# Optimization experiments

Measured on AMD Instinct MI355X. Metric: run time of the kernel, lower is better.

## Reference

```python
import jax, jax.numpy as jnp
import numpy as np

PAD_IDX, EOS_IDX, SOS_IDX = 0, 1, 2
NEG = -10000.0


def setup_inputs() -> dict:
    key = jax.random.key(0)
    k1, k2, k3 = jax.random.split(key, 3)
    B, T, K = 64, 2048, 256
    y = jax.random.normal(k1, (B, T, K), dtype=jnp.float32)
    # transition matrix initialized as in crf.__init__
    trans = jax.random.normal(k2, (K, K), dtype=jnp.float32)
    trans = trans.at[SOS_IDX, :].set(NEG)
    trans = trans.at[:, EOS_IDX].set(NEG)
    trans = trans.at[:, PAD_IDX].set(NEG)
    trans = trans.at[PAD_IDX, :].set(NEG)
    trans = trans.at[PAD_IDX, EOS_IDX].set(0.0)
    trans = trans.at[PAD_IDX, PAD_IDX].set(0.0)
    # variable-length float mask (1.0 for valid steps), as the module expects
    lengths = jax.random.randint(k3, (B,), T // 2, T + 1)
    mask = (jnp.arange(T)[None, :] < lengths[:, None]).astype(jnp.float32)
    return {"y": y, "mask": mask, "trans": trans}


def reference(y, mask, trans):
    # Linear-chain CRF partition function (forward algorithm in log space).
    # new_score[b,i] = y[b,t,i] + logsumexp_j(score[b,j] + trans[i,j])
    B, T, K = y.shape
    score0 = jnp.full((B, K), NEG, dtype=y.dtype).at[:, SOS_IDX].set(0.0)

    def step(score, xs):
        emit_t, mask_t = xs  # [B,K], [B]
        # score[b,None,j] + trans[None,i,j] -> lse over j
        new = emit_t + jax.scipy.special.logsumexp(
            score[:, None, :] + trans[None, :, :], axis=-1)
        m = mask_t[:, None]
        score = new * m + score * (1.0 - m)
        return score, None

    score, _ = jax.lax.scan(step, score0,
                            (jnp.swapaxes(y, 0, 1), mask.T))  # scan over T
    return jax.scipy.special.logsumexp(score, axis=-1)  # [B]
```

## Files before the change

kernel.cpp:

```cpp
#include <hip/hip_runtime.h>


typedef _Float16 f16x8 __attribute__((ext_vector_type(8)));
typedef _Float16 f16x4 __attribute__((ext_vector_type(4)));
typedef float    f32x4 __attribute__((ext_vector_type(4)));

#define TT 2048
#define KK 256
#define NB 16
#define NTH 512
#define SOS_IDX 2

#define MFMA(A, B, C) __builtin_amdgcn_mfma_f32_16x16x32_f16((A), (B), (C), 0, 0, 0)

__global__ __launch_bounds__(NTH, 2)
void crf_fwd_kernel(const float* __restrict__ y, const float* __restrict__ mask,
                    const float* __restrict__ trans, float* __restrict__ out)
{
    const int tid = threadIdx.x;
    const int w = tid >> 6, l = tid & 63;
    const int c = l & 15;
    const int s = l >> 4;
    const int sw = (c & 7) << 4;
    const int bb = blockIdx.x * NB;

    __shared__ __align__(16) char  Vlds[2][NB * 512];
    __shared__ __align__(16) float sred[2][NB][12];
    __shared__ float Lcs[NB];

    f16x8 af0[8], af1[8];
    {
        const float* t0 = trans + (size_t)(32 * w + c) * KK + 8 * s;
        const float* t1 = t0 + 16 * KK;
        #pragma unroll
        for (int kt = 0; kt < 8; ++kt) {
            float4 a0 = *(const float4*)(t0 + 32 * kt);
            float4 a1 = *(const float4*)(t0 + 32 * kt + 4);
            float4 b0 = *(const float4*)(t1 + 32 * kt);
            float4 b1 = *(const float4*)(t1 + 32 * kt + 4);
            f16x8 A, Bv;
            A[0] = (_Float16)__expf(a0.x); A[1] = (_Float16)__expf(a0.y);
            A[2] = (_Float16)__expf(a0.z); A[3] = (_Float16)__expf(a0.w);
            A[4] = (_Float16)__expf(a1.x); A[5] = (_Float16)__expf(a1.y);
            A[6] = (_Float16)__expf(a1.z); A[7] = (_Float16)__expf(a1.w);
            Bv[0] = (_Float16)__expf(b0.x); Bv[1] = (_Float16)__expf(b0.y);
            Bv[2] = (_Float16)__expf(b0.z); Bv[3] = (_Float16)__expf(b0.w);
            Bv[4] = (_Float16)__expf(b1.x); Bv[5] = (_Float16)__expf(b1.y);
            Bv[6] = (_Float16)__expf(b1.z); Bv[7] = (_Float16)__expf(b1.w);
            af0[kt] = A; af1[kt] = Bv;
        }
    }

    {
        const int cq = tid >> 5, q = tid & 31;
        const float* mrow = mask + (size_t)(bb + cq) * TT;
        float ls = 0.f;
        #pragma unroll
        for (int i = 0; i < TT / 32; ++i) ls += mrow[q + 32 * i];
        #pragma unroll
        for (int off = 16; off >= 1; off >>= 1) ls += __shfl_xor(ls, off, 64);
        if (q == 0) Lcs[cq] = ls;
    }

    const int r0 = 32 * w + 4 * s;
    float W0 = (r0 + 0 == SOS_IDX) ? 1.f : 0.f;
    float W1 = (r0 + 1 == SOS_IDX) ? 1.f : 0.f;
    float W2 = (r0 + 2 == SOS_IDX) ? 1.f : 0.f;
    float W3 = (r0 + 3 == SOS_IDX) ? 1.f : 0.f;
    float W4 = (r0 + 16 == SOS_IDX) ? 1.f : 0.f;
    float W5 = (r0 + 17 == SOS_IDX) ? 1.f : 0.f;
    float W6 = (r0 + 18 == SOS_IDX) ? 1.f : 0.f;
    float W7 = (r0 + 19 == SOS_IDX) ? 1.f : 0.f;
    {
        char* wb = Vlds[0] + (c << 9);
        f16x4 h0 = {(_Float16)W0, (_Float16)W1, (_Float16)W2, (_Float16)W3};
        f16x4 h1 = {(_Float16)W4, (_Float16)W5, (_Float16)W6, (_Float16)W7};
        *(f16x4*)(wb + ((64 * w + 8 * s) ^ sw))      = h0;
        *(f16x4*)(wb + ((64 * w + 32 + 8 * s) ^ sw)) = h1;
        float ps = ((W0 + W1) + (W2 + W3)) + ((W4 + W5) + (W6 + W7));
        ps += __shfl_xor(ps, 16, 64);
        ps += __shfl_xor(ps, 32, 64);
        if (s == 0) sred[0][c][w] = ps;
    }
    __syncthreads();

    float Tm = 0.f;
    #pragma unroll
    for (int i = 0; i < NB; ++i) Tm = fmaxf(Tm, Lcs[i]);
    const int Tmax = (int)(Tm + 0.5f);
    const int Lci  = (int)(Lcs[c] + 0.5f);

    const float* yb = y + (size_t)(bb + c) * (TT * KK) + 32 * w + 4 * s;
    float4 yA0 = *(const float4*)(yb);
    float4 yA1 = *(const float4*)(yb + 16);
    const int t1i = (Tmax > 1) ? 1 : 0;
    float4 yB0 = *(const float4*)(yb + (size_t)t1i * KK);
    float4 yB1 = *(const float4*)(yb + (size_t)t1i * KK + 16);
    float Lam = 0.f;

#define STEP(PAR, Y0, Y1, TS)                                                    \
  {                                                                              \
    const int t_ = (TS);                                                         \
    const char* vb = Vlds[PAR] + (c << 9);                                       \
    f16x8 b0 = *(const f16x8*)(vb + ((0   + (s << 4)) ^ sw));                    \
    f16x8 b1 = *(const f16x8*)(vb + ((64  + (s << 4)) ^ sw));                    \
    f16x8 b2 = *(const f16x8*)(vb + ((128 + (s << 4)) ^ sw));                    \
    f16x8 b3 = *(const f16x8*)(vb + ((192 + (s << 4)) ^ sw));                    \
    f16x8 b4 = *(const f16x8*)(vb + ((256 + (s << 4)) ^ sw));                    \
    f16x8 b5 = *(const f16x8*)(vb + ((320 + (s << 4)) ^ sw));                    \
    f16x8 b6 = *(const f16x8*)(vb + ((384 + (s << 4)) ^ sw));                    \
    f16x8 b7 = *(const f16x8*)(vb + ((448 + (s << 4)) ^ sw));                    \
    float4 sp0 = *(const float4*)&sred[PAR][c][0];                               \
    float4 sp1 = *(const float4*)&sred[PAR][c][4];                               \
    float Sg = ((sp0.x + sp0.y) + (sp0.z + sp0.w)) +                             \
               ((sp1.x + sp1.y) + (sp1.z + sp1.w));                              \
    float g  = 0.03125f * __builtin_amdgcn_rcpf(Sg);                             \
    float lg = __log2f(Sg);                                                      \
    f32x4 zz = {0.f, 0.f, 0.f, 0.f};                                             \
    f32x4 c0a = zz, c0b = zz, c1a = zz, c1b = zz;                                \
    c0a = MFMA(af0[0], b0, c0a); c1a = MFMA(af1[0], b0, c1a);                    \
    c0b = MFMA(af0[4], b4, c0b); c1b = MFMA(af1[4], b4, c1b);                    \
    c0a = MFMA(af0[1], b1, c0a); c1a = MFMA(af1[1], b1, c1a);                    \
    c0b = MFMA(af0[5], b5, c0b); c1b = MFMA(af1[5], b5, c1b);                    \
    c0a = MFMA(af0[2], b2, c0a); c1a = MFMA(af1[2], b2, c1a);                    \
    c0b = MFMA(af0[6], b6, c0b); c1b = MFMA(af1[6], b6, c1b);                    \
    c0a = MFMA(af0[3], b3, c0a); c1a = MFMA(af1[3], b3, c1a);                    \
    c0b = MFMA(af0[7], b7, c0b); c1b = MFMA(af1[7], b7, c1b);                    \
    const bool on = (t_ < Lci);                                                  \
    f32x4 q0 = c0a + c0b, q1 = c1a + c1b;                                        \
    float n0 = on ? __expf(Y0.x) * q0[0] * g : W0;                               \
    float n1 = on ? __expf(Y0.y) * q0[1] * g : W1;                               \
    float n2 = on ? __expf(Y0.z) * q0[2] * g : W2;                               \
    float n3 = on ? __expf(Y0.w) * q0[3] * g : W3;                               \
    float n4 = on ? __expf(Y1.x) * q1[0] * g : W4;                               \
    float n5 = on ? __expf(Y1.y) * q1[1] * g : W5;                               \
    float n6 = on ? __expf(Y1.z) * q1[2] * g : W6;                               \
    float n7 = on ? __expf(Y1.w) * q1[3] * g : W7;                               \
    W0 = n0; W1 = n1; W2 = n2; W3 = n3; W4 = n4; W5 = n5; W6 = n6; W7 = n7;      \
    Lam += on ? lg : 0.f;                                                        \
    char* wb = Vlds[(PAR) ^ 1] + (c << 9);                                       \
    f16x4 h0 = {(_Float16)n0, (_Float16)n1, (_Float16)n2, (_Float16)n3};         \
    f16x4 h1 = {(_Float16)n4, (_Float16)n5, (_Float16)n6, (_Float16)n7};         \
    *(f16x4*)(wb + ((64 * w + 8 * s) ^ sw))      = h0;                           \
    *(f16x4*)(wb + ((64 * w + 32 + 8 * s) ^ sw)) = h1;                           \
    float ps = ((n0 + n1) + (n2 + n3)) + ((n4 + n5) + (n6 + n7));                \
    ps += __shfl_xor(ps, 16, 64);                                                \
    ps += __shfl_xor(ps, 32, 64);                                                \
    if (s == 0) sred[(PAR) ^ 1][c][w] = ps;                                      \
    { int tn = t_ + 2; if (tn > Tmax - 1) tn = Tmax - 1;                         \
      Y0 = *(const float4*)(yb + (size_t)tn * KK);                               \
      Y1 = *(const float4*)(yb + (size_t)tn * KK + 16); }                        \
    asm volatile("s_waitcnt lgkmcnt(0)" ::: "memory");                           \
    __builtin_amdgcn_s_barrier();                                                \
    __builtin_amdgcn_sched_barrier(0);                                           \
  }

    int t = 0;
    for (; t + 1 < Tmax; t += 2) {
        STEP(0, yA0, yA1, t);
        STEP(1, yB0, yB1, t + 1);
    }
    if (t < Tmax) STEP(0, yA0, yA1, t);

#undef STEP

    if (tid < NB) {
        const int fin = Tmax & 1;
        float Sf = 0.f;
        #pragma unroll
        for (int i = 0; i < 8; ++i) Sf += sred[fin][tid][i];
        out[bb + tid] = 0.69314718056f * (Lam + __log2f(Sf) + 5.0f * (float)Lci);
    }
}

extern "C" void kernel_launch(void* const* d_in, const int* in_sizes, int n_in,
                              void* d_out, int out_size, void* d_ws, size_t ws_size,
                              hipStream_t stream) {
    const float* y     = (const float*)d_in[0];
    const float* mask  = (const float*)d_in[1];
    const float* trans = (const float*)d_in[2];
    float* out = (float*)d_out;
    const int B = in_sizes[1] / TT;
    crf_fwd_kernel<<<B / NB, NTH, 0, stream>>>(y, mask, trans, out);
}
```

Before: 1.482 ms.

## Compute normalizer from fp16 LDS vector, fold scale into exp2 argument

Each wave now recomputes the sum of the previous state vector directly from the fp16 values it already loads from LDS for the MFMA, instead of a separate shared-memory partial-sum array written and reduced per step. The normalization (including the 1/32 factor) is folded into the exponent as exp2(y*log2e - 5 - log2 S) using the raw hardware exp instruction, which removes the reciprocal and extra multiplies. The MFMA chain is split into four independent accumulators per output tile for more instruction-level parallelism, and the fp16 stores use packed round-toward-zero conversion. The sum is now taken in fp16 over rounded values, so there is a risk of overflow or lost precision.

```diff
diff --git a/kernel.cpp b/kernel.cpp
--- a/kernel.cpp
+++ b/kernel.cpp
@@ -2,7 +2,8 @@
 
 
 typedef _Float16 f16x8 __attribute__((ext_vector_type(8)));
-typedef _Float16 f16x4 __attribute__((ext_vector_type(4)));
+typedef _Float16 f16x2 __attribute__((ext_vector_type(2)));
+typedef __fp16   fp16x2 __attribute__((ext_vector_type(2)));
 typedef float    f32x4 __attribute__((ext_vector_type(4)));
 
 #define TT 2048
@@ -12,6 +13,14 @@
 #define SOS_IDX 2
 
 #define MFMA(A, B, C) __builtin_amdgcn_mfma_f32_16x16x32_f16((A), (B), (C), 0, 0, 0)
+
+static __device__ __forceinline__ float exp2_hw(float x) {
+    float r; asm("v_exp_f32 %0, %1" : "=v"(r) : "v"(x)); return r;
+}
+static __device__ __forceinline__ unsigned pkrtz(float a, float b) {
+    fp16x2 h = __builtin_amdgcn_cvt_pkrtz(a, b);
+    return __builtin_bit_cast(unsigned, h);
+}
 
 __global__ __launch_bounds__(NTH, 2)
 void crf_fwd_kernel(const float* __restrict__ y, const float* __restrict__ mask,
@@ -25,7 +34,6 @@
     const int bb = blockIdx.x * NB;
 
     __shared__ __align__(16) char  Vlds[2][NB * 512];
-    __shared__ __align__(16) float sred[2][NB][12];
     __shared__ float Lcs[NB];
 
     f16x8 af0[8], af1[8];
@@ -73,14 +81,8 @@
     float W7 = (r0 + 19 == SOS_IDX) ? 1.f : 0.f;
     {
         char* wb = Vlds[0] + (c << 9);
-        f16x4 h0 = {(_Float16)W0, (_Float16)W1, (_Float16)W2, (_Float16)W3};
-        f16x4 h1 = {(_Float16)W4, (_Float16)W5, (_Float16)W6, (_Float16)W7};
-        *(f16x4*)(wb + ((64 * w + 8 * s) ^ sw))      = h0;
-        *(f16x4*)(wb + ((64 * w + 32 + 8 * s) ^ sw)) = h1;
-        float ps = ((W0 + W1) + (W2 + W3)) + ((W4 + W5) + (W6 + W7));
-        ps += __shfl_xor(ps, 16, 64);
-        ps += __shfl_xor(ps, 32, 64);
-        if (s == 0) sred[0][c][w] = ps;
+        *(uint2*)(wb + ((64 * w + 8 * s) ^ sw))      = make_uint2(pkrtz(W0, W1), pkrtz(W2, W3));
+        *(uint2*)(wb + ((64 * w + 32 + 8 * s) ^ sw)) = make_uint2(pkrtz(W4, W5), pkrtz(W6, W7));
     }
     __syncthreads();
 
@@ -110,43 +112,44 @@
     f16x8 b5 = *(const f16x8*)(vb + ((320 + (s << 4)) ^ sw));                    \
     f16x8 b6 = *(const f16x8*)(vb + ((384 + (s << 4)) ^ sw));                    \
     f16x8 b7 = *(const f16x8*)(vb + ((448 + (s << 4)) ^ sw));                    \
-    float4 sp0 = *(const float4*)&sred[PAR][c][0];                               \
-    float4 sp1 = *(const float4*)&sred[PAR][c][4];                               \
-    float Sg = ((sp0.x + sp0.y) + (sp0.z + sp0.w)) +                             \
-               ((sp1.x + sp1.y) + (sp1.z + sp1.w));                              \
-    float g  = 0.03125f * __builtin_amdgcn_rcpf(Sg);                             \
-    float lg = __log2f(Sg);                                                      \
+    f16x8 ta = (b0 + b1) + (b2 + b3);                                            \
+    f16x8 tb = (b4 + b5) + (b6 + b7);                                            \
+    f16x8 tc = ta + tb;                                                          \
+    f16x2 u0 = {tc[0], tc[1]}, u1 = {tc[2], tc[3]};                              \
+    f16x2 u2 = {tc[4], tc[5]}, u3 = {tc[6], tc[7]};                              \
+    f16x2 uu = (u0 + u1) + (u2 + u3);                                            \
+    float Sl = (float)uu[0] + (float)uu[1];                                      \
+    Sl += __shfl_xor(Sl, 16, 64);                                                \
+    Sl += __shfl_xor(Sl, 32, 64);                                                \
+    float lS  = __log2f(Sl);                                                     \
+    float lgg = -5.0f - lS;                                                      \
     f32x4 zz = {0.f, 0.f, 0.f, 0.f};                                             \
-    f32x4 c0a = zz, c0b = zz, c1a = zz, c1b = zz;                                \
+    f32x4 c0a = zz, c0b = zz, c0c = zz, c0d = zz;                                \
+    f32x4 c1a = zz, c1b = zz, c1c = zz, c1d = zz;                                \
     c0a = MFMA(af0[0], b0, c0a); c1a = MFMA(af1[0], b0, c1a);                    \
-    c0b = MFMA(af0[4], b4, c0b); c1b = MFMA(af1[4], b4, c1b);                    \
+    c0b = MFMA(af0[2], b2, c0b); c1b = MFMA(af1[2], b2, c1b);                    \
+    c0c = MFMA(af0[4], b4, c0c); c1c = MFMA(af1[4], b4, c1c);                    \
+    c0d = MFMA(af0[6], b6, c0d); c1d = MFMA(af1[6], b6, c1d);                    \
     c0a = MFMA(af0[1], b1, c0a); c1a = MFMA(af1[1], b1, c1a);                    \
-    c0b = MFMA(af0[5], b5, c0b); c1b = MFMA(af1[5], b5, c1b);                    \
-    c0a = MFMA(af0[2], b2, c0a); c1a = MFMA(af1[2], b2, c1a);                    \
-    c0b = MFMA(af0[6], b6, c0b); c1b = MFMA(af1[6], b6, c1b);                    \
-    c0a = MFMA(af0[3], b3, c0a); c1a = MFMA(af1[3], b3, c1a);                    \
-    c0b = MFMA(af0[7], b7, c0b); c1b = MFMA(af1[7], b7, c1b);                    \
+    c0b = MFMA(af0[3], b3, c0b); c1b = MFMA(af1[3], b3, c1b);                    \
+    c0c = MFMA(af0[5], b5, c0c); c1c = MFMA(af1[5], b5, c1c);                    \
+    c0d = MFMA(af0[7], b7, c0d); c1d = MFMA(af1[7], b7, c1d);                    \
     const bool on = (t_ < Lci);                                                  \
-    f32x4 q0 = c0a + c0b, q1 = c1a + c1b;                                        \
-    float n0 = on ? __expf(Y0.x) * q0[0] * g : W0;                               \
-    float n1 = on ? __expf(Y0.y) * q0[1] * g : W1;                               \
-    float n2 = on ? __expf(Y0.z) * q0[2] * g : W2;                               \
-    float n3 = on ? __expf(Y0.w) * q0[3] * g : W3;                               \
-    float n4 = on ? __expf(Y1.x) * q1[0] * g : W4;                               \
-    float n5 = on ? __expf(Y1.y) * q1[1] * g : W5;                               \
-    float n6 = on ? __expf(Y1.z) * q1[2] * g : W6;                               \
-    float n7 = on ? __expf(Y1.w) * q1[3] * g : W7;                               \
+    f32x4 q0 = (c0a + c0b) + (c0c + c0d);                                        \
+    f32x4 q1 = (c1a + c1b) + (c1c + c1d);                                        \
+    float n0 = on ? exp2_hw(fmaf(Y0.x, 1.44269504f, lgg)) * q0[0] : W0;          \
+    float n1 = on ? exp2_hw(fmaf(Y0.y, 1.44269504f, lgg)) * q0[1] : W1;          \
+    float n2 = on ? exp2_hw(fmaf(Y0.z, 1.44269504f, lgg)) * q0[2] : W2;          \
+    float n3 = on ? exp2_hw(fmaf(Y0.w, 1.44269504f, lgg)) * q0[3] : W3;          \
+    float n4 = on ? exp2_hw(fmaf(Y1.x, 1.44269504f, lgg)) * q1[0] : W4;          \
+    float n5 = on ? exp2_hw(fmaf(Y1.y, 1.44269504f, lgg)) * q1[1] : W5;          \
+    float n6 = on ? exp2_hw(fmaf(Y1.z, 1.44269504f, lgg)) * q1[2] : W6;          \
+    float n7 = on ? exp2_hw(fmaf(Y1.w, 1.44269504f, lgg)) * q1[3] : W7;          \
     W0 = n0; W1 = n1; W2 = n2; W3 = n3; W4 = n4; W5 = n5; W6 = n6; W7 = n7;      \
-    Lam += on ? lg : 0.f;                                                        \
+    Lam += on ? lS : 0.f;                                                        \
     char* wb = Vlds[(PAR) ^ 1] + (c << 9);                                       \
-    f16x4 h0 = {(_Float16)n0, (_Float16)n1, (_Float16)n2, (_Float16)n3};         \
-    f16x4 h1 = {(_Float16)n4, (_Float16)n5, (_Float16)n6, (_Float16)n7};         \
-    *(f16x4*)(wb + ((64 * w + 8 * s) ^ sw))      = h0;                           \
-    *(f16x4*)(wb + ((64 * w + 32 + 8 * s) ^ sw)) = h1;                           \
-    float ps = ((n0 + n1) + (n2 + n3)) + ((n4 + n5) + (n6 + n7));                \
-    ps += __shfl_xor(ps, 16, 64);                                                \
-    ps += __shfl_xor(ps, 32, 64);                                                \
-    if (s == 0) sred[(PAR) ^ 1][c][w] = ps;                                      \
+    *(uint2*)(wb + ((64 * w + 8 * s) ^ sw))      = make_uint2(pkrtz(n0, n1), pkrtz(n2, n3)); \
+    *(uint2*)(wb + ((64 * w + 32 + 8 * s) ^ sw)) = make_uint2(pkrtz(n4, n5), pkrtz(n6, n7)); \
     { int tn = t_ + 2; if (tn > Tmax - 1) tn = Tmax - 1;                         \
       Y0 = *(const float4*)(yb + (size_t)tn * KK);                               \
       Y1 = *(const float4*)(yb + (size_t)tn * KK + 16); }                        \
@@ -164,12 +167,25 @@
 
 #undef STEP
 
-    if (tid < NB) {
-        const int fin = Tmax & 1;
-        float Sf = 0.f;
-        #pragma unroll
-        for (int i = 0; i < 8; ++i) Sf += sred[fin][tid][i];
-        out[bb + tid] = 0.69314718056f * (Lam + __log2f(Sf) + 5.0f * (float)Lci);
+    if (w == 0) {
+        const char* vb = Vlds[Tmax & 1] + (c << 9);
+        f16x8 b0 = *(const f16x8*)(vb + ((0   + (s << 4)) ^ sw));
+        f16x8 b1 = *(const f16x8*)(vb + ((64  + (s << 4)) ^ sw));
+        f16x8 b2 = *(const f16x8*)(vb + ((128 + (s << 4)) ^ sw));
+        f16x8 b3 = *(const f16x8*)(vb + ((192 + (s << 4)) ^ sw));
+        f16x8 b4 = *(const f16x8*)(vb + ((256 + (s << 4)) ^ sw));
+        f16x8 b5 = *(const f16x8*)(vb + ((320 + (s << 4)) ^ sw));
+        f16x8 b6 = *(const f16x8*)(vb + ((384 + (s << 4)) ^ sw));
+        f16x8 b7 = *(const f16x8*)(vb + ((448 + (s << 4)) ^ sw));
+        f16x8 tc = ((b0 + b1) + (b2 + b3)) + ((b4 + b5) + (b6 + b7));
+        f16x2 u0 = {tc[0], tc[1]}, u1 = {tc[2], tc[3]};
+        f16x2 u2 = {tc[4], tc[5]}, u3 = {tc[6], tc[7]};
+        f16x2 uu = (u0 + u1) + (u2 + u3);
+        float Sf = (float)uu[0] + (float)uu[1];
+        Sf += __shfl_xor(Sf, 16, 64);
+        Sf += __shfl_xor(Sf, 32, 64);
+        if (l < 16)
+            out[bb + c] = 0.69314718056f * (Lam + __log2f(Sf) + 5.0f * (float)Lci);
     }
 }
 
```

New measurement: 1.826 ms. +23.2%, slower.

## Interleave two independent 16-sequence chains per block and compute normaliser from LDS

Applied to the files above, without the earlier changes.

Each block now processes 32 batch sequences as two independent groups (A and B), so each barrier-separated step carries two independent MFMA chains and elementwise updates that can overlap. The per-step normaliser is no longer passed through a separate shared reduction buffer. It is recomputed from the f16 state vector loaded for the MFMA, summed in half precision and combined with shuffles. This halves the number of barriers per sequence but launches only 2 blocks instead of 4, using fewer CUs. It also adds register pressure and fp16 rounding in the normaliser sum.

```diff
diff --git a/kernel.cpp b/kernel.cpp
--- a/kernel.cpp
+++ b/kernel.cpp
@@ -3,11 +3,11 @@
 
 typedef _Float16 f16x8 __attribute__((ext_vector_type(8)));
 typedef _Float16 f16x4 __attribute__((ext_vector_type(4)));
+typedef _Float16 f16x2 __attribute__((ext_vector_type(2)));
 typedef float    f32x4 __attribute__((ext_vector_type(4)));
 
 #define TT 2048
 #define KK 256
-#define NB 16
 #define NTH 512
 #define SOS_IDX 2
 
@@ -22,11 +22,11 @@
     const int c = l & 15;
     const int s = l >> 4;
     const int sw = (c & 7) << 4;
-    const int bb = blockIdx.x * NB;
-
-    __shared__ __align__(16) char  Vlds[2][NB * 512];
-    __shared__ __align__(16) float sred[2][NB][12];
-    __shared__ float Lcs[NB];
+    const int bb = blockIdx.x * 32;
+
+    __shared__ __align__(16) char VA[2][16 * 512];
+    __shared__ __align__(16) char VB[2][16 * 512];
+    __shared__ float Lcs[32];
 
     f16x8 af0[8], af1[8];
     {
@@ -52,104 +52,168 @@
     }
 
     {
-        const int cq = tid >> 5, q = tid & 31;
+        const int cq = tid >> 4, q = tid & 15;
         const float* mrow = mask + (size_t)(bb + cq) * TT;
         float ls = 0.f;
         #pragma unroll
-        for (int i = 0; i < TT / 32; ++i) ls += mrow[q + 32 * i];
+        for (int i = 0; i < TT / 16; ++i) ls += mrow[q + 16 * i];
         #pragma unroll
-        for (int off = 16; off >= 1; off >>= 1) ls += __shfl_xor(ls, off, 64);
+        for (int off = 8; off >= 1; off >>= 1) ls += __shfl_xor(ls, off, 64);
         if (q == 0) Lcs[cq] = ls;
     }
 
     const int r0 = 32 * w + 4 * s;
-    float W0 = (r0 + 0 == SOS_IDX) ? 1.f : 0.f;
-    float W1 = (r0 + 1 == SOS_IDX) ? 1.f : 0.f;
-    float W2 = (r0 + 2 == SOS_IDX) ? 1.f : 0.f;
-    float W3 = (r0 + 3 == SOS_IDX) ? 1.f : 0.f;
-    float W4 = (r0 + 16 == SOS_IDX) ? 1.f : 0.f;
-    float W5 = (r0 + 17 == SOS_IDX) ? 1.f : 0.f;
-    float W6 = (r0 + 18 == SOS_IDX) ? 1.f : 0.f;
-    float W7 = (r0 + 19 == SOS_IDX) ? 1.f : 0.f;
+    float WA0 = (r0 + 0 == SOS_IDX) ? 1.f : 0.f;
+    float WA1 = (r0 + 1 == SOS_IDX) ? 1.f : 0.f;
+    float WA2 = (r0 + 2 == SOS_IDX) ? 1.f : 0.f;
+    float WA3 = (r0 + 3 == SOS_IDX) ? 1.f : 0.f;
+    float WA4 = (r0 + 16 == SOS_IDX) ? 1.f : 0.f;
+    float WA5 = (r0 + 17 == SOS_IDX) ? 1.f : 0.f;
+    float WA6 = (r0 + 18 == SOS_IDX) ? 1.f : 0.f;
+    float WA7 = (r0 + 19 == SOS_IDX) ? 1.f : 0.f;
+    float WB0 = WA0, WB1 = WA1, WB2 = WA2, WB3 = WA3;
+    float WB4 = WA4, WB5 = WA5, WB6 = WA6, WB7 = WA7;
     {
-        char* wb = Vlds[0] + (c << 9);
-        f16x4 h0 = {(_Float16)W0, (_Float16)W1, (_Float16)W2, (_Float16)W3};
-        f16x4 h1 = {(_Float16)W4, (_Float16)W5, (_Float16)W6, (_Float16)W7};
+        f16x4 h0 = {(_Float16)WA0, (_Float16)WA1, (_Float16)WA2, (_Float16)WA3};
+        f16x4 h1 = {(_Float16)WA4, (_Float16)WA5, (_Float16)WA6, (_Float16)WA7};
+        char* wa = VA[0] + (c << 9);
+        char* wb = VB[0] + (c << 9);
+        *(f16x4*)(wa + ((64 * w + 8 * s) ^ sw))      = h0;
+        *(f16x4*)(wa + ((64 * w + 32 + 8 * s) ^ sw)) = h1;
         *(f16x4*)(wb + ((64 * w + 8 * s) ^ sw))      = h0;
         *(f16x4*)(wb + ((64 * w + 32 + 8 * s) ^ sw)) = h1;
-        float ps = ((W0 + W1) + (W2 + W3)) + ((W4 + W5) + (W6 + W7));
-        ps += __shfl_xor(ps, 16, 64);
-        ps += __shfl_xor(ps, 32, 64);
-        if (s == 0) sred[0][c][w] = ps;
     }
     __syncthreads();
 
     float Tm = 0.f;
     #pragma unroll
-    for (int i = 0; i < NB; ++i) Tm = fmaxf(Tm, Lcs[i]);
+    for (int i = 0; i < 32; ++i) Tm = fmaxf(Tm, Lcs[i]);
     const int Tmax = (int)(Tm + 0.5f);
-    const int Lci  = (int)(Lcs[c] + 0.5f);
-
-    const float* yb = y + (size_t)(bb + c) * (TT * KK) + 32 * w + 4 * s;
-    float4 yA0 = *(const float4*)(yb);
-    float4 yA1 = *(const float4*)(yb + 16);
+    const int LciA = (int)(Lcs[c] + 0.5f);
+    const int LciB = (int)(Lcs[16 + c] + 0.5f);
+
+    const float* ybA = y + (size_t)(bb + c) * (TT * KK) + 32 * w + 4 * s;
+    const float* ybB = ybA + (size_t)16 * TT * KK;
+    float4 yAa0 = *(const float4*)(ybA);
+    float4 yAa1 = *(const float4*)(ybA + 16);
+    float4 yBa0 = *(const float4*)(ybB);
+    float4 yBa1 = *(const float4*)(ybB + 16);
     const int t1i = (Tmax > 1) ? 1 : 0;
-    float4 yB0 = *(const float4*)(yb + (size_t)t1i * KK);
-    float4 yB1 = *(const float4*)(yb + (size_t)t1i * KK + 16);
-    float Lam = 0.f;
-
-#define STEP(PAR, Y0, Y1, TS)                                                    \
+    float4 yAb0 = *(const float4*)(ybA + (size_t)t1i * KK);
+    float4 yAb1 = *(const float4*)(ybA + (size_t)t1i * KK + 16);
+    float4 yBb0 = *(const float4*)(ybB + (size_t)t1i * KK);
+    float4 yBb1 = *(const float4*)(ybB + (size_t)t1i * KK + 16);
+    float LamA = 0.f, LamB = 0.f;
+
+#define INTERVAL(PAR, YA0, YA1, YB0, YB1, TS)                                    \
   {                                                                              \
     const int t_ = (TS);                                                         \
-    const char* vb = Vlds[PAR] + (c << 9);                                       \
-    f16x8 b0 = *(const f16x8*)(vb + ((0   + (s << 4)) ^ sw));                    \
-    f16x8 b1 = *(const f16x8*)(vb + ((64  + (s << 4)) ^ sw));                    \
-    f16x8 b2 = *(const f16x8*)(vb + ((128 + (s << 4)) ^ sw));                    \
-    f16x8 b3 = *(const f16x8*)(vb + ((192 + (s << 4)) ^ sw));                    \
-    f16x8 b4 = *(const f16x8*)(vb + ((256 + (s << 4)) ^ sw));                    \
-    f16x8 b5 = *(const f16x8*)(vb + ((320 + (s << 4)) ^ sw));                    \
-    f16x8 b6 = *(const f16x8*)(vb + ((384 + (s << 4)) ^ sw));                    \
-    f16x8 b7 = *(const f16x8*)(vb + ((448 + (s << 4)) ^ sw));                    \
-    float4 sp0 = *(const float4*)&sred[PAR][c][0];                               \
-    float4 sp1 = *(const float4*)&sred[PAR][c][4];                               \
-    float Sg = ((sp0.x + sp0.y) + (sp0.z + sp0.w)) +                             \
-               ((sp1.x + sp1.y) + (sp1.z + sp1.w));                              \
-    float g  = 0.03125f * __builtin_amdgcn_rcpf(Sg);                             \
-    float lg = __log2f(Sg);                                                      \
+                                             \
+    const char* va_ = VA[PAR] + (c << 9);                                        \
+    f16x8 a0 = *(const f16x8*)(va_ + ((0   + (s << 4)) ^ sw));                   \
+    f16x8 a1 = *(const f16x8*)(va_ + ((64  + (s << 4)) ^ sw));                   \
+    f16x8 a2 = *(const f16x8*)(va_ + ((128 + (s << 4)) ^ sw));                   \
+    f16x8 a3 = *(const f16x8*)(va_ + ((192 + (s << 4)) ^ sw));                   \
+    f16x8 a4 = *(const f16x8*)(va_ + ((256 + (s << 4)) ^ sw));                   \
+    f16x8 a5 = *(const f16x8*)(va_ + ((320 + (s << 4)) ^ sw));                   \
+    f16x8 a6 = *(const f16x8*)(va_ + ((384 + (s << 4)) ^ sw));                   \
+    f16x8 a7 = *(const f16x8*)(va_ + ((448 + (s << 4)) ^ sw));                   \
     f32x4 zz = {0.f, 0.f, 0.f, 0.f};                                             \
-    f32x4 c0a = zz, c0b = zz, c1a = zz, c1b = zz;                                \
-    c0a = MFMA(af0[0], b0, c0a); c1a = MFMA(af1[0], b0, c1a);                    \
-    c0b = MFMA(af0[4], b4, c0b); c1b = MFMA(af1[4], b4, c1b);                    \
-    c0a = MFMA(af0[1], b1, c0a); c1a = MFMA(af1[1], b1, c1a);                    \
-    c0b = MFMA(af0[5], b5, c0b); c1b = MFMA(af1[5], b5, c1b);                    \
-    c0a = MFMA(af0[2], b2, c0a); c1a = MFMA(af1[2], b2, c1a);                    \
-    c0b = MFMA(af0[6], b6, c0b); c1b = MFMA(af1[6], b6, c1b);                    \
-    c0a = MFMA(af0[3], b3, c0a); c1a = MFMA(af1[3], b3, c1a);                    \
-    c0b = MFMA(af0[7], b7, c0b); c1b = MFMA(af1[7], b7, c1b);                    \
-    const bool on = (t_ < Lci);                                                  \
-    f32x4 q0 = c0a + c0b, q1 = c1a + c1b;                                        \
-    float n0 = on ? __expf(Y0.x) * q0[0] * g : W0;                               \
-    float n1 = on ? __expf(Y0.y) * q0[1] * g : W1;                               \
-    float n2 = on ? __expf(Y0.z) * q0[2] * g : W2;                               \
-    float n3 = on ? __expf(Y0.w) * q0[3] * g : W3;                               \
-    float n4 = on ? __expf(Y1.x) * q1[0] * g : W4;                               \
-    float n5 = on ? __expf(Y1.y) * q1[1] * g : W5;                               \
-    float n6 = on ? __expf(Y1.z) * q1[2] * g : W6;                               \
-    float n7 = on ? __expf(Y1.w) * q1[3] * g : W7;                               \
-    W0 = n0; W1 = n1; W2 = n2; W3 = n3; W4 = n4; W5 = n5; W6 = n6; W7 = n7;      \
-    Lam += on ? lg : 0.f;                                                        \
-    char* wb = Vlds[(PAR) ^ 1] + (c << 9);                                       \
-    f16x4 h0 = {(_Float16)n0, (_Float16)n1, (_Float16)n2, (_Float16)n3};         \
-    f16x4 h1 = {(_Float16)n4, (_Float16)n5, (_Float16)n6, (_Float16)n7};         \
-    *(f16x4*)(wb + ((64 * w + 8 * s) ^ sw))      = h0;                           \
-    *(f16x4*)(wb + ((64 * w + 32 + 8 * s) ^ sw)) = h1;                           \
-    float ps = ((n0 + n1) + (n2 + n3)) + ((n4 + n5) + (n6 + n7));                \
-    ps += __shfl_xor(ps, 16, 64);                                                \
-    ps += __shfl_xor(ps, 32, 64);                                                \
-    if (s == 0) sred[(PAR) ^ 1][c][w] = ps;                                      \
+    f32x4 cA0a = zz, cA0b = zz, cA1a = zz, cA1b = zz;                            \
+    cA0a = MFMA(af0[0], a0, cA0a); cA1a = MFMA(af1[0], a0, cA1a);                \
+    cA0b = MFMA(af0[4], a4, cA0b); cA1b = MFMA(af1[4], a4, cA1b);                \
+    cA0a = MFMA(af0[1], a1, cA0a); cA1a = MFMA(af1[1], a1, cA1a);                \
+    cA0b = MFMA(af0[5], a5, cA0b); cA1b = MFMA(af1[5], a5, cA1b);                \
+    cA0a = MFMA(af0[2], a2, cA0a); cA1a = MFMA(af1[2], a2, cA1a);                \
+    cA0b = MFMA(af0[6], a6, cA0b); cA1b = MFMA(af1[6], a6, cA1b);                \
+    cA0a = MFMA(af0[3], a3, cA0a); cA1a = MFMA(af1[3], a3, cA1a);                \
+    cA0b = MFMA(af0[7], a7, cA0b); cA1b = MFMA(af1[7], a7, cA1b);                \
+               \
+    f16x8 tA = ((a0 + a1) + (a2 + a3)) + ((a4 + a5) + (a6 + a7));                \
+    f16x2 uA0 = {tA[0], tA[1]}, uA1 = {tA[2], tA[3]};                            \
+    f16x2 uA2 = {tA[4], tA[5]}, uA3 = {tA[6], tA[7]};                            \
+    f16x2 uuA = (uA0 + uA1) + (uA2 + uA3);                                       \
+    float SgA = (float)uuA[0] + (float)uuA[1];                                   \
+    SgA += __shfl_xor(SgA, 16, 64);                                              \
+    SgA += __shfl_xor(SgA, 32, 64);                                              \
+    float gA  = 0.03125f * __builtin_amdgcn_rcpf(SgA);                           \
+    float lgA = __log2f(SgA);                                                    \
+                                             \
+    const char* vb_ = VB[PAR] + (c << 9);                                        \
+    f16x8 b0 = *(const f16x8*)(vb_ + ((0   + (s << 4)) ^ sw));                   \
+    f16x8 b1 = *(const f16x8*)(vb_ + ((64  + (s << 4)) ^ sw));                   \
+    f16x8 b2 = *(const f16x8*)(vb_ + ((128 + (s << 4)) ^ sw));                   \
+    f16x8 b3 = *(const f16x8*)(vb_ + ((192 + (s << 4)) ^ sw));                   \
+    f16x8 b4 = *(const f16x8*)(vb_ + ((256 + (s << 4)) ^ sw));                   \
+    f16x8 b5 = *(const f16x8*)(vb_ + ((320 + (s << 4)) ^ sw));                   \
+    f16x8 b6 = *(const f16x8*)(vb_ + ((384 + (s << 4)) ^ sw));                   \
+    f16x8 b7 = *(const f16x8*)(vb_ + ((448 + (s << 4)) ^ sw));                   \
+    f32x4 cB0a = zz, cB0b = zz, cB1a = zz, cB1b = zz;                            \
+    cB0a = MFMA(af0[0], b0, cB0a); cB1a = MFMA(af1[0], b0, cB1a);                \
+    cB0b = MFMA(af0[4], b4, cB0b); cB1b = MFMA(af1[4], b4, cB1b);                \
+    cB0a = MFMA(af0[1], b1, cB0a); cB1a = MFMA(af1[1], b1, cB1a);                \
+    cB0b = MFMA(af0[5], b5, cB0b); cB1b = MFMA(af1[5], b5, cB1b);                \
+    cB0a = MFMA(af0[2], b2, cB0a); cB1a = MFMA(af1[2], b2, cB1a);                \
+    cB0b = MFMA(af0[6], b6, cB0b); cB1b = MFMA(af1[6], b6, cB1b);                \
+    cB0a = MFMA(af0[3], b3, cB0a); cB1a = MFMA(af1[3], b3, cB1a);                \
+    cB0b = MFMA(af0[7], b7, cB0b); cB1b = MFMA(af1[7], b7, cB1b);                \
+    f16x8 tB = ((b0 + b1) + (b2 + b3)) + ((b4 + b5) + (b6 + b7));                \
+    f16x2 uB0 = {tB[0], tB[1]}, uB1 = {tB[2], tB[3]};                            \
+    f16x2 uB2 = {tB[4], tB[5]}, uB3 = {tB[6], tB[7]};                            \
+    f16x2 uuB = (uB0 + uB1) + (uB2 + uB3);                                       \
+    float SgB = (float)uuB[0] + (float)uuB[1];                                   \
+    SgB += __shfl_xor(SgB, 16, 64);                                              \
+    SgB += __shfl_xor(SgB, 32, 64);                                              \
+    float gB  = 0.03125f * __builtin_amdgcn_rcpf(SgB);                           \
+    float lgB = __log2f(SgB);                                                    \
+             \
+    const bool onA = (t_ < LciA);                                                \
+    f32x4 qA0 = cA0a + cA0b, qA1 = cA1a + cA1b;                                  \
+    float nA0 = onA ? __expf(YA0.x) * qA0[0] * gA : WA0;                         \
+    float nA1 = onA ? __expf(YA0.y) * qA0[1] * gA : WA1;                         \
+    float nA2 = onA ? __expf(YA0.z) * qA0[2] * gA : WA2;                         \
+    float nA3 = onA ? __expf(YA0.w) * qA0[3] * gA : WA3;                         \
+    float nA4 = onA ? __expf(YA1.x) * qA1[0] * gA : WA4;                         \
+    float nA5 = onA ? __expf(YA1.y) * qA1[1] * gA : WA5;                         \
+    float nA6 = onA ? __expf(YA1.z) * qA1[2] * gA : WA6;                         \
+    float nA7 = onA ? __expf(YA1.w) * qA1[3] * gA : WA7;                         \
+    WA0 = nA0; WA1 = nA1; WA2 = nA2; WA3 = nA3;                                  \
+    WA4 = nA4; WA5 = nA5; WA6 = nA6; WA7 = nA7;                                  \
+    LamA += onA ? lgA : 0.f;                                                     \
+    {                                                                            \
+      char* wp = VA[(PAR) ^ 1] + (c << 9);                                       \
+      f16x4 h0 = {(_Float16)nA0, (_Float16)nA1, (_Float16)nA2, (_Float16)nA3};   \
+      f16x4 h1 = {(_Float16)nA4, (_Float16)nA5, (_Float16)nA6, (_Float16)nA7};   \
+      *(f16x4*)(wp + ((64 * w + 8 * s) ^ sw))      = h0;                         \
+      *(f16x4*)(wp + ((64 * w + 32 + 8 * s) ^ sw)) = h1;                         \
+    }                                                                            \
     { int tn = t_ + 2; if (tn > Tmax - 1) tn = Tmax - 1;                         \
-      Y0 = *(const float4*)(yb + (size_t)tn * KK);                               \
-      Y1 = *(const float4*)(yb + (size_t)tn * KK + 16); }                        \
+      YA0 = *(const float4*)(ybA + (size_t)tn * KK);                             \
+      YA1 = *(const float4*)(ybA + (size_t)tn * KK + 16); }                      \
+                                                       \
+    const bool onB = (t_ < LciB);                                                \
+    f32x4 qB0 = cB0a + cB0b, qB1 = cB1a + cB1b;                                  \
+    float nB0 = onB ? __expf(YB0.x) * qB0[0] * gB : WB0;                         \
+    float nB1 = onB ? __expf(YB0.y) * qB0[1] * gB : WB1;                         \
+    float nB2 = onB ? __expf(YB0.z) * qB0[2] * gB : WB2;                         \
+    float nB3 = onB ? __expf(YB0.w) * qB0[3] * gB : WB3;                         \
+    float nB4 = onB ? __expf(YB1.x) * qB1[0] * gB : WB4;                         \
+    float nB5 = onB ? __expf(YB1.y) * qB1[1] * gB : WB5;                         \
+    float nB6 = onB ? __expf(YB1.z) * qB1[2] * gB : WB6;                         \
+    float nB7 = onB ? __expf(YB1.w) * qB1[3] * gB : WB7;                         \
+    WB0 = nB0; WB1 = nB1; WB2 = nB2; WB3 = nB3;                                  \
+    WB4 = nB4; WB5 = nB5; WB6 = nB6; WB7 = nB7;                                  \
+    LamB += onB ? lgB : 0.f;                                                     \
+    {                                                                            \
+      char* wp = VB[(PAR) ^ 1] + (c << 9);                                       \
+      f16x4 h0 = {(_Float16)nB0, (_Float16)nB1, (_Float16)nB2, (_Float16)nB3};   \
+      f16x4 h1 = {(_Float16)nB4, (_Float16)nB5, (_Float16)nB6, (_Float16)nB7};   \
+      *(f16x4*)(wp + ((64 * w + 8 * s) ^ sw))      = h0;                         \
+      *(f16x4*)(wp + ((64 * w + 32 + 8 * s) ^ sw)) = h1;                         \
+    }                                                                            \
+    { int tn = t_ + 2; if (tn > Tmax - 1) tn = Tmax - 1;                         \
+      YB0 = *(const float4*)(ybB + (size_t)tn * KK);                             \
+      YB1 = *(const float4*)(ybB + (size_t)tn * KK + 16); }                      \
     asm volatile("s_waitcnt lgkmcnt(0)" ::: "memory");                           \
     __builtin_amdgcn_s_barrier();                                                \
     __builtin_amdgcn_sched_barrier(0);                                           \
@@ -157,19 +221,52 @@
 
     int t = 0;
     for (; t + 1 < Tmax; t += 2) {
-        STEP(0, yA0, yA1, t);
-        STEP(1, yB0, yB1, t + 1);
-    }
-    if (t < Tmax) STEP(0, yA0, yA1, t);
-
-#undef STEP
-
-    if (tid < NB) {
-        const int fin = Tmax & 1;
-        float Sf = 0.f;
-        #pragma unroll
-        for (int i = 0; i < 8; ++i) Sf += sred[fin][tid][i];
-        out[bb + tid] = 0.69314718056f * (Lam + __log2f(Sf) + 5.0f * (float)Lci);
+        INTERVAL(0, yAa0, yAa1, yBa0, yBa1, t);
+        INTERVAL(1, yAb0, yAb1, yBb0, yBb1, t + 1);
+    }
+    if (t < Tmax) INTERVAL(0, yAa0, yAa1, yBa0, yBa1, t);
+
+#undef INTERVAL
+
+    const int fin = Tmax & 1;
+    if (w == 0) {
+        const char* vp = VA[fin] + (c << 9);
+        f16x8 e0 = *(const f16x8*)(vp + ((0   + (s << 4)) ^ sw));
+        f16x8 e1 = *(const f16x8*)(vp + ((64  + (s << 4)) ^ sw));
+        f16x8 e2 = *(const f16x8*)(vp + ((128 + (s << 4)) ^ sw));
+        f16x8 e3 = *(const f16x8*)(vp + ((192 + (s << 4)) ^ sw));
+        f16x8 e4 = *(const f16x8*)(vp + ((256 + (s << 4)) ^ sw));
+        f16x8 e5 = *(const f16x8*)(vp + ((320 + (s << 4)) ^ sw));
+        f16x8 e6 = *(const f16x8*)(vp + ((384 + (s << 4)) ^ sw));
+        f16x8 e7 = *(const f16x8*)(vp + ((448 + (s << 4)) ^ sw));
+        f16x8 tc = ((e0 + e1) + (e2 + e3)) + ((e4 + e5) + (e6 + e7));
+        f16x2 u0 = {tc[0], tc[1]}, u1 = {tc[2], tc[3]};
+        f16x2 u2 = {tc[4], tc[5]}, u3 = {tc[6], tc[7]};
+        f16x2 uu = (u0 + u1) + (u2 + u3);
+        float Sf = (float)uu[0] + (float)uu[1];
+        Sf += __shfl_xor(Sf, 16, 64);
+        Sf += __shfl_xor(Sf, 32, 64);
+        if (l < 16)
+            out[bb + c] = 0.69314718056f * (LamA + __log2f(Sf) + 5.0f * (float)LciA);
+    } else if (w == 1) {
+        const char* vp = VB[fin] + (c << 9);
+        f16x8 e0 = *(const f16x8*)(vp + ((0   + (s << 4)) ^ sw));
+        f16x8 e1 = *(const f16x8*)(vp + ((64  + (s << 4)) ^ sw));
+        f16x8 e2 = *(const f16x8*)(vp + ((128 + (s << 4)) ^ sw));
+        f16x8 e3 = *(const f16x8*)(vp + ((192 + (s << 4)) ^ sw));
+        f16x8 e4 = *(const f16x8*)(vp + ((256 + (s << 4)) ^ sw));
+        f16x8 e5 = *(const f16x8*)(vp + ((320 + (s << 4)) ^ sw));
+        f16x8 e6 = *(const f16x8*)(vp + ((384 + (s << 4)) ^ sw));
+        f16x8 e7 = *(const f16x8*)(vp + ((448 + (s << 4)) ^ sw));
+        f16x8 tc = ((e0 + e1) + (e2 + e3)) + ((e4 + e5) + (e6 + e7));
+        f16x2 u0 = {tc[0], tc[1]}, u1 = {tc[2], tc[3]};
+        f16x2 u2 = {tc[4], tc[5]}, u3 = {tc[6], tc[7]};
+        f16x2 uu = (u0 + u1) + (u2 + u3);
+        float Sf = (float)uu[0] + (float)uu[1];
+        Sf += __shfl_xor(Sf, 16, 64);
+        Sf += __shfl_xor(Sf, 32, 64);
+        if (l < 16)
+            out[bb + 16 + c] = 0.69314718056f * (LamB + __log2f(Sf) + 5.0f * (float)LciB);
     }
 }
 
@@ -181,5 +278,5 @@
     const float* trans = (const float*)d_in[2];
     float* out = (float*)d_out;
     const int B = in_sizes[1] / TT;
-    crf_fwd_kernel<<<B / NB, NTH, 0, stream>>>(y, mask, trans, out);
+    crf_fwd_kernel<<<B / 32, NTH, 0, stream>>>(y, mask, trans, out);
 }
```

After: 3.219 ms. 117% more time.
